# Kernel optimization log

Hardware: AMD Instinct MI355X
Metric: run time of the kernel (lower is better)

## Reference

```python
import jax, jax.numpy as jnp
import numpy as np

BATCH = 8192
MAX_ATOMS = 512  # angles_max_length


def setup_inputs() -> dict:
    key = jax.random.key(0)
    k1, k2, k3 = jax.random.split(key, 3)
    inp = jax.random.normal(k1, (BATCH, 3 * MAX_ATOMS), dtype=jnp.float32)
    tgt = jax.random.normal(k2, (BATCH, 3 * MAX_ATOMS), dtype=jnp.float32)
    num_atoms = jax.random.randint(k3, (BATCH,), 0, MAX_ATOMS, dtype=jnp.int64)
    num_atoms = jnp.maximum(num_atoms, 16)  # avoid degenerate tiny structures
    return {"input": inp, "target": tgt, "num_atoms": num_atoms}


def _kabsch_rmsd(inp, tgt, num_atoms):
    B = inp.shape[0]
    N = inp.shape[1] // 3
    src = inp.reshape(B, N, 3)
    dst = tgt.reshape(B, N, 3)
    # mask out padding atoms
    mask = (jnp.arange(N)[None, :] < num_atoms[:, None])[..., None]  # [B,N,1]
    n = num_atoms.astype(inp.dtype)[:, None, None]                   # [B,1,1]
    src = jnp.where(mask, src, 0.0)
    dst = jnp.where(dst.dtype.type(0) == 0, jnp.where(mask, dst, 0.0), dst)
    # center on masked centroid, re-zero padding
    src_c = jnp.where(mask, src - jnp.sum(src, axis=1, keepdims=True) / n, 0.0)
    dst_c = jnp.where(mask, dst - jnp.sum(dst, axis=1, keepdims=True) / n, 0.0)
    # 3x3 correlation matrices
    R = jnp.einsum("bni,bnj->bij", src_c, dst_c)  # [B,3,3]
    U, S, Vt = jnp.linalg.svd(R)
    d = jnp.sign(jnp.linalg.det(U) * jnp.linalg.det(Vt))  # chirality correction
    trace_opt = S[:, 0] + S[:, 1] + d * S[:, 2]
    sq = jnp.sum(src_c * src_c, axis=(1, 2)) + jnp.sum(dst_c * dst_c, axis=(1, 2))
    na = num_atoms.astype(inp.dtype)
    msd = (sq - 2.0 * trace_opt) / na
    return jnp.sqrt(jnp.clip(msd, 0.0))


def reference(input, target, num_atoms):
    return _kabsch_rmsd(input, target, num_atoms)
```

## Files before the change

kernel.cpp:

```cpp
#include <hip/hip_runtime.h>
#include <math.h>

#define NATOMS 512
#define TPB 256
#define WPB 4

__global__ __launch_bounds__(TPB) void kabsch_rmsd_kernel(
    const float* __restrict__ inp,
    const float* __restrict__ tgt,
    const int* __restrict__ num_atoms,
    float* __restrict__ out,
    int B)
{
    const int wave = threadIdx.x >> 6;
    const int lane = threadIdx.x & 63;
    const int b = blockIdx.x * WPB + wave;
    if (b >= B) return;

    const int na = num_atoms[b];

    const float4* s4 = (const float4*)(inp + (size_t)b * (3 * NATOMS)) + 6 * lane;
    const float4* d4 = (const float4*)(tgt + (size_t)b * (3 * NATOMS)) + 6 * lane;

    union U { float4 q[6]; float f[24]; };
    U S, D;
    #pragma unroll
    for (int i = 0; i < 6; ++i) S.q[i] = s4[i];
    #pragma unroll
    for (int i = 0; i < 6; ++i) D.q[i] = d4[i];

    float v[16];
    #pragma unroll
    for (int i = 0; i < 16; ++i) v[i] = 0.f;

    const int base = lane * 8;
    #pragma unroll
    for (int k = 0; k < 8; ++k) {
        const float m = (base + k < na) ? 1.f : 0.f;
        const float sx = S.f[3 * k]     * m;
        const float sy = S.f[3 * k + 1] * m;
        const float sz = S.f[3 * k + 2] * m;
        const float dx = D.f[3 * k]     * m;
        const float dy = D.f[3 * k + 1] * m;
        const float dz = D.f[3 * k + 2] * m;
        v[0]  += sx * dx;  v[1]  += sx * dy;  v[2]  += sx * dz;
        v[3]  += sy * dx;  v[4]  += sy * dy;  v[5]  += sy * dz;
        v[6]  += sz * dx;  v[7]  += sz * dy;  v[8]  += sz * dz;
        v[9]  += sx;  v[10] += sy;  v[11] += sz;
        v[12] += dx;  v[13] += dy;  v[14] += dz;
        v[15] += sx * sx + sy * sy + sz * sz + dx * dx + dy * dy + dz * dz;
    }

    #pragma unroll
    for (int i = 0; i < 16; ++i) {
        #pragma unroll
        for (int mask = 32; mask > 0; mask >>= 1) {
            v[i] += __shfl_xor(v[i], mask);
        }
    }

    if (lane == 0) {
        const double n = (double)na;
        const double sx = (double)v[9],  sy = (double)v[10], sz = (double)v[11];
        const double tx = (double)v[12], ty = (double)v[13], tz = (double)v[14];

        double R[3][3];
        R[0][0] = (double)v[0] - sx * tx / n;
        R[0][1] = (double)v[1] - sx * ty / n;
        R[0][2] = (double)v[2] - sx * tz / n;
        R[1][0] = (double)v[3] - sy * tx / n;
        R[1][1] = (double)v[4] - sy * ty / n;
        R[1][2] = (double)v[5] - sy * tz / n;
        R[2][0] = (double)v[6] - sz * tx / n;
        R[2][1] = (double)v[7] - sz * ty / n;
        R[2][2] = (double)v[8] - sz * tz / n;

        const double sq = (double)v[15] - (sx * sx + sy * sy + sz * sz
                                         + tx * tx + ty * ty + tz * tz) / n;

        const double detR =
            R[0][0] * (R[1][1] * R[2][2] - R[1][2] * R[2][1])
          - R[0][1] * (R[1][0] * R[2][2] - R[1][2] * R[2][0])
          + R[0][2] * (R[1][0] * R[2][1] - R[1][1] * R[2][0]);

        double A00 = R[0][0]*R[0][0] + R[1][0]*R[1][0] + R[2][0]*R[2][0];
        double A11 = R[0][1]*R[0][1] + R[1][1]*R[1][1] + R[2][1]*R[2][1];
        double A22 = R[0][2]*R[0][2] + R[1][2]*R[1][2] + R[2][2]*R[2][2];
        double A01 = R[0][0]*R[0][1] + R[1][0]*R[1][1] + R[2][0]*R[2][1];
        double A02 = R[0][0]*R[0][2] + R[1][0]*R[1][2] + R[2][0]*R[2][2];
        double A12 = R[0][1]*R[0][2] + R[1][1]*R[1][2] + R[2][1]*R[2][2];

        double e0, e1, e2;
        const double p1 = A01*A01 + A02*A02 + A12*A12;
        if (p1 < 1e-30) {
            e0 = A00; e1 = A11; e2 = A22;
            double tmp;
            if (e0 < e1) { tmp = e0; e0 = e1; e1 = tmp; }
            if (e1 < e2) { tmp = e1; e1 = e2; e2 = tmp; }
            if (e0 < e1) { tmp = e0; e0 = e1; e1 = tmp; }
        } else {
            const double q  = (A00 + A11 + A22) / 3.0;
            const double b00 = A00 - q, b11 = A11 - q, b22 = A22 - q;
            const double p2 = b00*b00 + b11*b11 + b22*b22 + 2.0 * p1;
            const double p  = sqrt(p2 / 6.0);
            const double ip = 1.0 / p;
            const double B00 = b00*ip, B11 = b11*ip, B22 = b22*ip;
            const double B01 = A01*ip, B02 = A02*ip, B12 = A12*ip;
            double r = 0.5 * (B00 * (B11 * B22 - B12 * B12)
                            - B01 * (B01 * B22 - B12 * B02)
                            + B02 * (B01 * B12 - B11 * B02));
            if (r < -1.0) r = -1.0;
            if (r >  1.0) r =  1.0;
            const double phi = acos(r) / 3.0;
            e0 = q + 2.0 * p * cos(phi);
            e2 = q + 2.0 * p * cos(phi + 2.0943951023931953);
            e1 = 3.0 * q - e0 - e2;
        }

        const double S0 = sqrt(e0 > 0.0 ? e0 : 0.0);
        const double S1 = sqrt(e1 > 0.0 ? e1 : 0.0);
        const double S2 = sqrt(e2 > 0.0 ? e2 : 0.0);
        const double dsgn = (detR > 0.0) ? 1.0 : ((detR < 0.0) ? -1.0 : 0.0);
        const double trace_opt = S0 + S1 + dsgn * S2;

        double msd = (sq - 2.0 * trace_opt) / n;
        if (msd < 0.0) msd = 0.0;
        out[b] = (float)sqrt(msd);
    }
}

extern "C" void kernel_launch(void* const* d_in, const int* in_sizes, int n_in,
                              void* d_out, int out_size, void* d_ws, size_t ws_size,
                              hipStream_t stream) {
    const float* inp = (const float*)d_in[0];
    const float* tgt = (const float*)d_in[1];
    const int* num_atoms = (const int*)d_in[2];
    float* out = (float*)d_out;

    const int B = in_sizes[0] / (3 * NATOMS);
    const int blocks = (B + WPB - 1) / WPB;
    kabsch_rmsd_kernel<<<blocks, TPB, 0, stream>>>(inp, tgt, num_atoms, out, B);
}
```

Measured before the change: 124.4 us.

## Split reduction and fp64 eigen epilogue into two kernels via workspace

Splits the fused kernel in two. The first kernel reduces the per-structure sums and writes 16 partial floats per batch element to workspace. The second kernel runs the double-precision eigenvalue/SVD epilogue with one thread per structure, so it is no longer executed serially by lane 0 of each wave while the other 63 lanes sit idle. The cost is a second launch and a small round trip of partials through global memory.

Result: no change. 122.1 us (-1.8%).

```diff
diff --git a/kernel.cpp b/kernel.cpp
--- a/kernel.cpp
+++ b/kernel.cpp
@@ -4,12 +4,13 @@
 #define NATOMS 512
 #define TPB 256
 #define WPB 4
+#define FPE (3 * NATOMS)
 
-__global__ __launch_bounds__(TPB) void kabsch_rmsd_kernel(
+__global__ __launch_bounds__(TPB) void kabsch_reduce_kernel(
     const float* __restrict__ inp,
     const float* __restrict__ tgt,
     const int* __restrict__ num_atoms,
-    float* __restrict__ out,
+    float* __restrict__ partial,
     int B)
 {
     const int wave = threadIdx.x >> 6;
@@ -19,8 +20,8 @@
 
     const int na = num_atoms[b];
 
-    const float4* s4 = (const float4*)(inp + (size_t)b * (3 * NATOMS)) + 6 * lane;
-    const float4* d4 = (const float4*)(tgt + (size_t)b * (3 * NATOMS)) + 6 * lane;
+    const float4* s4 = (const float4*)(inp + (size_t)b * FPE) + 6 * lane;
+    const float4* d4 = (const float4*)(tgt + (size_t)b * FPE) + 6 * lane;
 
     union U { float4 q[6]; float f[24]; };
     U S, D;
@@ -60,73 +61,97 @@
     }
 
     if (lane == 0) {
-        const double n = (double)na;
-        const double sx = (double)v[9],  sy = (double)v[10], sz = (double)v[11];
-        const double tx = (double)v[12], ty = (double)v[13], tz = (double)v[14];
+        float4* p = (float4*)(partial + (size_t)b * 16);
+        p[0] = make_float4(v[0],  v[1],  v[2],  v[3]);
+        p[1] = make_float4(v[4],  v[5],  v[6],  v[7]);
+        p[2] = make_float4(v[8],  v[9],  v[10], v[11]);
+        p[3] = make_float4(v[12], v[13], v[14], v[15]);
+    }
+}
 
-        double R[3][3];
-        R[0][0] = (double)v[0] - sx * tx / n;
-        R[0][1] = (double)v[1] - sx * ty / n;
-        R[0][2] = (double)v[2] - sx * tz / n;
-        R[1][0] = (double)v[3] - sy * tx / n;
-        R[1][1] = (double)v[4] - sy * ty / n;
-        R[1][2] = (double)v[5] - sy * tz / n;
-        R[2][0] = (double)v[6] - sz * tx / n;
-        R[2][1] = (double)v[7] - sz * ty / n;
-        R[2][2] = (double)v[8] - sz * tz / n;
+__global__ __launch_bounds__(TPB) void kabsch_epilogue_kernel(
+    const float* __restrict__ partial,
+    const int* __restrict__ num_atoms,
+    float* __restrict__ out,
+    int B)
+{
+    const int b = blockIdx.x * TPB + threadIdx.x;
+    if (b >= B) return;
 
-        const double sq = (double)v[15] - (sx * sx + sy * sy + sz * sz
-                                         + tx * tx + ty * ty + tz * tz) / n;
+    const float4* p = (const float4*)(partial + (size_t)b * 16);
+    const float4 r0 = p[0], r1 = p[1], r2 = p[2], r3 = p[3];
+    float v[16] = { r0.x, r0.y, r0.z, r0.w,
+                    r1.x, r1.y, r1.z, r1.w,
+                    r2.x, r2.y, r2.z, r2.w,
+                    r3.x, r3.y, r3.z, r3.w };
 
-        const double detR =
-            R[0][0] * (R[1][1] * R[2][2] - R[1][2] * R[2][1])
-          - R[0][1] * (R[1][0] * R[2][2] - R[1][2] * R[2][0])
-          + R[0][2] * (R[1][0] * R[2][1] - R[1][1] * R[2][0]);
+    const int na = num_atoms[b];
+    const double n = (double)na;
+    const double sx = (double)v[9],  sy = (double)v[10], sz = (double)v[11];
+    const double tx = (double)v[12], ty = (double)v[13], tz = (double)v[14];
 
-        double A00 = R[0][0]*R[0][0] + R[1][0]*R[1][0] + R[2][0]*R[2][0];
-        double A11 = R[0][1]*R[0][1] + R[1][1]*R[1][1] + R[2][1]*R[2][1];
-        double A22 = R[0][2]*R[0][2] + R[1][2]*R[1][2] + R[2][2]*R[2][2];
-        double A01 = R[0][0]*R[0][1] + R[1][0]*R[1][1] + R[2][0]*R[2][1];
-        double A02 = R[0][0]*R[0][2] + R[1][0]*R[1][2] + R[2][0]*R[2][2];
-        double A12 = R[0][1]*R[0][2] + R[1][1]*R[1][2] + R[2][1]*R[2][2];
+    double R[3][3];
+    R[0][0] = (double)v[0] - sx * tx / n;
+    R[0][1] = (double)v[1] - sx * ty / n;
+    R[0][2] = (double)v[2] - sx * tz / n;
+    R[1][0] = (double)v[3] - sy * tx / n;
+    R[1][1] = (double)v[4] - sy * ty / n;
+    R[1][2] = (double)v[5] - sy * tz / n;
+    R[2][0] = (double)v[6] - sz * tx / n;
+    R[2][1] = (double)v[7] - sz * ty / n;
+    R[2][2] = (double)v[8] - sz * tz / n;
 
-        double e0, e1, e2;
-        const double p1 = A01*A01 + A02*A02 + A12*A12;
-        if (p1 < 1e-30) {
-            e0 = A00; e1 = A11; e2 = A22;
-            double tmp;
-            if (e0 < e1) { tmp = e0; e0 = e1; e1 = tmp; }
-            if (e1 < e2) { tmp = e1; e1 = e2; e2 = tmp; }
-            if (e0 < e1) { tmp = e0; e0 = e1; e1 = tmp; }
-        } else {
-            const double q  = (A00 + A11 + A22) / 3.0;
-            const double b00 = A00 - q, b11 = A11 - q, b22 = A22 - q;
-            const double p2 = b00*b00 + b11*b11 + b22*b22 + 2.0 * p1;
-            const double p  = sqrt(p2 / 6.0);
-            const double ip = 1.0 / p;
-            const double B00 = b00*ip, B11 = b11*ip, B22 = b22*ip;
-            const double B01 = A01*ip, B02 = A02*ip, B12 = A12*ip;
-            double r = 0.5 * (B00 * (B11 * B22 - B12 * B12)
-                            - B01 * (B01 * B22 - B12 * B02)
-                            + B02 * (B01 * B12 - B11 * B02));
-            if (r < -1.0) r = -1.0;
-            if (r >  1.0) r =  1.0;
-            const double phi = acos(r) / 3.0;
-            e0 = q + 2.0 * p * cos(phi);
-            e2 = q + 2.0 * p * cos(phi + 2.0943951023931953);
-            e1 = 3.0 * q - e0 - e2;
-        }
+    const double sq = (double)v[15] - (sx * sx + sy * sy + sz * sz
+                                     + tx * tx + ty * ty + tz * tz) / n;
 
-        const double S0 = sqrt(e0 > 0.0 ? e0 : 0.0);
-        const double S1 = sqrt(e1 > 0.0 ? e1 : 0.0);
-        const double S2 = sqrt(e2 > 0.0 ? e2 : 0.0);
-        const double dsgn = (detR > 0.0) ? 1.0 : ((detR < 0.0) ? -1.0 : 0.0);
-        const double trace_opt = S0 + S1 + dsgn * S2;
+    const double detR =
+        R[0][0] * (R[1][1] * R[2][2] - R[1][2] * R[2][1])
+      - R[0][1] * (R[1][0] * R[2][2] - R[1][2] * R[2][0])
+      + R[0][2] * (R[1][0] * R[2][1] - R[1][1] * R[2][0]);
 
-        double msd = (sq - 2.0 * trace_opt) / n;
-        if (msd < 0.0) msd = 0.0;
-        out[b] = (float)sqrt(msd);
+    double A00 = R[0][0]*R[0][0] + R[1][0]*R[1][0] + R[2][0]*R[2][0];
+    double A11 = R[0][1]*R[0][1] + R[1][1]*R[1][1] + R[2][1]*R[2][1];
+    double A22 = R[0][2]*R[0][2] + R[1][2]*R[1][2] + R[2][2]*R[2][2];
+    double A01 = R[0][0]*R[0][1] + R[1][0]*R[1][1] + R[2][0]*R[2][1];
+    double A02 = R[0][0]*R[0][2] + R[1][0]*R[1][2] + R[2][0]*R[2][2];
+    double A12 = R[0][1]*R[0][2] + R[1][1]*R[1][2] + R[2][1]*R[2][2];
+
+    double e0, e1, e2;
+    const double p1 = A01*A01 + A02*A02 + A12*A12;
+    if (p1 < 1e-30) {
+        e0 = A00; e1 = A11; e2 = A22;
+        double tmp;
+        if (e0 < e1) { tmp = e0; e0 = e1; e1 = tmp; }
+        if (e1 < e2) { tmp = e1; e1 = e2; e2 = tmp; }
+        if (e0 < e1) { tmp = e0; e0 = e1; e1 = tmp; }
+    } else {
+        const double q  = (A00 + A11 + A22) / 3.0;
+        const double b00 = A00 - q, b11 = A11 - q, b22 = A22 - q;
+        const double p2 = b00*b00 + b11*b11 + b22*b22 + 2.0 * p1;
+        const double pp = sqrt(p2 / 6.0);
+        const double ip = 1.0 / pp;
+        const double B00 = b00*ip, B11 = b11*ip, B22 = b22*ip;
+        const double B01 = A01*ip, B02 = A02*ip, B12 = A12*ip;
+        double r = 0.5 * (B00 * (B11 * B22 - B12 * B12)
+                        - B01 * (B01 * B22 - B12 * B02)
+                        + B02 * (B01 * B12 - B11 * B02));
+        if (r < -1.0) r = -1.0;
+        if (r >  1.0) r =  1.0;
+        const double phi = acos(r) / 3.0;
+        e0 = q + 2.0 * pp * cos(phi);
+        e2 = q + 2.0 * pp * cos(phi + 2.0943951023931953);
+        e1 = 3.0 * q - e0 - e2;
     }
+
+    const double S0 = sqrt(e0 > 0.0 ? e0 : 0.0);
+    const double S1 = sqrt(e1 > 0.0 ? e1 : 0.0);
+    const double S2 = sqrt(e2 > 0.0 ? e2 : 0.0);
+    const double dsgn = (detR > 0.0) ? 1.0 : ((detR < 0.0) ? -1.0 : 0.0);
+    const double trace_opt = S0 + S1 + dsgn * S2;
+
+    double msd = (sq - 2.0 * trace_opt) / n;
+    if (msd < 0.0) msd = 0.0;
+    out[b] = (float)sqrt(msd);
 }
 
 extern "C" void kernel_launch(void* const* d_in, const int* in_sizes, int n_in,
@@ -136,8 +161,11 @@
     const float* tgt = (const float*)d_in[1];
     const int* num_atoms = (const int*)d_in[2];
     float* out = (float*)d_out;
+    float* partial = (float*)d_ws;
 
-    const int B = in_sizes[0] / (3 * NATOMS);
-    const int blocks = (B + WPB - 1) / WPB;
-    kabsch_rmsd_kernel<<<blocks, TPB, 0, stream>>>(inp, tgt, num_atoms, out, B);
+    const int B = in_sizes[0] / FPE;
+    const int blocks1 = (B + WPB - 1) / WPB;
+    kabsch_reduce_kernel<<<blocks1, TPB, 0, stream>>>(inp, tgt, num_atoms, partial, B);
+    const int blocks2 = (B + TPB - 1) / TPB;
+    kabsch_epilogue_kernel<<<blocks2, TPB, 0, stream>>>(partial, num_atoms, out, B);
 }
```
